# Kernel optimization log

Measured on AMD Instinct MI355X. Metric: run time of the kernel, lower is better.

The kernel has to match this reference:

```python
import jax, jax.numpy as jnp
import numpy as np

D = 768
H = 12
DK = D // H
FF = 3072
EPS = 1e-5


def layernorm(x, g, b):
    mu = jnp.mean(x, axis=-1, keepdims=True)
    var = jnp.mean((x - mu) ** 2, axis=-1, keepdims=True)
    return (x - mu) * jax.lax.rsqrt(var + EPS) * g + b


def setup_inputs() -> dict:
    key = jax.random.key(0)
    ks = jax.random.split(key, 12)
    B, S = 4, 2048
    s = 0.02
    return {
        "embedding": jax.random.normal(ks[0], (B, S, D), jnp.float32),
        "mask": jnp.ones((B, 1, 1, S), jnp.int32),
        "Wq": jax.random.normal(ks[1], (D, D), jnp.float32) * s,
        "bq": jnp.zeros((D,), jnp.float32),
        "Wk": jax.random.normal(ks[2], (D, D), jnp.float32) * s,
        "bk": jnp.zeros((D,), jnp.float32),
        "Wv": jax.random.normal(ks[3], (D, D), jnp.float32) * s,
        "bv": jnp.zeros((D,), jnp.float32),
        "Wo": jax.random.normal(ks[4], (D, D), jnp.float32) * s,
        "bo": jnp.zeros((D,), jnp.float32),
        "W1": jax.random.normal(ks[5], (D, FF), jnp.float32) * s,
        "b1": jnp.zeros((FF,), jnp.float32),
        "W2": jax.random.normal(ks[6], (FF, D), jnp.float32) * s,
        "b2": jnp.zeros((D,), jnp.float32),
        "ln_g": jnp.ones((D,), jnp.float32),
        "ln_b": jnp.zeros((D,), jnp.float32),
    }


def reference(embedding, mask, Wq, bq, Wk, bk, Wv, bv, Wo, bo, W1, b1, W2, b2, ln_g, ln_b):
    B, S, _ = embedding.shape
    # QKV projections -> [B, H, S, DK]
    def split_heads(t):
        return t.reshape(B, S, H, DK).transpose(0, 2, 1, 3)
    q = split_heads(embedding @ Wq + bq)
    k = split_heads(embedding @ Wk + bk)
    v = split_heads(embedding @ Wv + bv)
    scores = jnp.einsum("bhqd,bhkd->bhqk", q, k) / jnp.sqrt(jnp.float32(DK))
    scores = jnp.where(mask == 0, jnp.float32(-1e9), scores)
    weights = jax.nn.softmax(scores, axis=-1)  # dropout = identity (eval)
    context = jnp.einsum("bhqk,bhkd->bhqd", weights, v)
    context = context.transpose(0, 2, 1, 3).reshape(B, S, D)
    attn_out = context @ Wo + bo
    x = layernorm(attn_out + embedding, ln_g, ln_b)
    ff = jax.nn.relu(x @ W1 + b1) @ W2 + b2
    return layernorm(x + ff, ln_g, ln_b)
```

## Files before the change

kernel.cpp:

```cpp
#include <hip/hip_runtime.h>

#define D_MODEL 768
#define NHEADS  12
#define SEQ     2048
#define BATCH   4
#define FF_DIM  3072
#define NTOK    (BATCH * SEQ)

typedef short short8 __attribute__((ext_vector_type(8)));
typedef float f32x4 __attribute__((ext_vector_type(4)));
typedef float f32x16 __attribute__((ext_vector_type(16)));
typedef int int4v __attribute__((ext_vector_type(4)));
typedef int int2v __attribute__((ext_vector_type(2)));
typedef unsigned short ushort4v __attribute__((ext_vector_type(4)));
typedef float float4v __attribute__((ext_vector_type(4)));

__device__ __forceinline__ short f2bf(float x) {
  unsigned u = __builtin_bit_cast(unsigned, x);
  u += 0x7fffu + ((u >> 16) & 1u);
  return (short)(u >> 16);
}
__device__ __forceinline__ float bf2f(short x) {
  return __builtin_bit_cast(float, ((unsigned)(unsigned short)x) << 16);
}
__device__ __forceinline__ int cvtpk(float a, float b) {
  int r;
  asm("v_cvt_pk_bf16_f32 %0, %1, %2" : "=v"(r) : "v"(a), "v"(b));
  return r;
}
__device__ __forceinline__ float fexp2(float x) {
#if __has_builtin(__builtin_amdgcn_exp2f)
  return __builtin_amdgcn_exp2f(x);
#else
  return exp2f(x);
#endif
}
__device__ __forceinline__ float frcp(float x) {
#if __has_builtin(__builtin_amdgcn_rcpf)
  return __builtin_amdgcn_rcpf(x);
#else
  return 1.f / x;
#endif
}
__device__ __forceinline__ void gll16(const void* g, void* l) {
  __builtin_amdgcn_global_load_lds(
      (const __attribute__((address_space(1))) void*)g,
      (__attribute__((address_space(3))) void*)l, 16, 0, 0);
}

__device__ __forceinline__ void wt_tile(float (*T)[65], const float* __restrict__ W,
                                        short* __restrict__ Wt, int K, int N,
                                        int bx, int by, int t) {
  const int c = t & 63, rb = t >> 6;
  const int k0 = by * 64, n0 = bx * 64;
#pragma unroll
  for (int i = 0; i < 16; ++i) {
    const int r = rb * 16 + i;
    T[c][r] = W[(size_t)(k0 + r) * N + n0 + c];
  }
  __syncthreads();
#pragma unroll
  for (int j = 0; j < 16; ++j) {
    const int idx = t + j * 256;
    const int nl = idx >> 6, kl = idx & 63;
    Wt[(size_t)(n0 + nl) * K + k0 + kl] = f2bf(T[nl][kl]);
  }
}

__global__ __launch_bounds__(256) void prep(
    const float* __restrict__ Wq, const float* __restrict__ Wk, const float* __restrict__ Wv,
    const float* __restrict__ Wo, const float* __restrict__ W1, const float* __restrict__ W2,
    const float* __restrict__ bq, const float* __restrict__ bk, const float* __restrict__ bv,
    const float* __restrict__ emb,
    short* __restrict__ wqkvt, short* __restrict__ wot, short* __restrict__ w1t,
    short* __restrict__ w2t, float* __restrict__ bqkv, short* __restrict__ x0) {
  __shared__ float T[64][65];
  const int bi = blockIdx.x;
  const int t = threadIdx.x;
  if (bi < 432) {
    const int s = bi / 144, l = bi % 144;
    const float* W = (s == 0) ? Wq : (s == 1) ? Wk : Wv;
    wt_tile(T, W, wqkvt + (size_t)s * 768 * 768, 768, 768, l % 12, l / 12, t);
  } else if (bi < 576) {
    const int l = bi - 432;
    wt_tile(T, Wo, wot, 768, 768, l % 12, l / 12, t);
  } else if (bi < 1152) {
    const int l = bi - 576;
    wt_tile(T, W1, w1t, 768, 3072, l % 48, l / 48, t);
  } else if (bi < 1728) {
    const int l = bi - 1152;
    wt_tile(T, W2, w2t, 3072, 768, l % 12, l / 12, t);
  } else if (bi == 1728) {
#pragma unroll
    for (int j = 0; j < 9; ++j) {
      const int i = t + j * 256;
      bqkv[i] = (i < 768) ? bq[i] : (i < 1536) ? bk[i - 768] : bv[i - 1536];
    }
  } else {
    const int i = (bi - 1729) * 256 + t;
    float4v v = *(const float4v*)(emb + (size_t)i * 4);
    ushort4v p;
    p[0] = (unsigned short)f2bf(v[0]);
    p[1] = (unsigned short)f2bf(v[1]);
    p[2] = (unsigned short)f2bf(v[2]);
    p[3] = (unsigned short)f2bf(v[3]);
    *(ushort4v*)(x0 + (size_t)i * 4) = p;
  }
}

enum { EPI_QKV = 0, EPI_WO = 1, EPI_RELU = 2, EPI_FF = 3 };

template <int EPI>
__global__ __launch_bounds__(256) void gemm_bt(const short* __restrict__ A,
                                               const short* __restrict__ Bt,
                                               const float* __restrict__ bias,
                                               const float* __restrict__ extraF,
                                               const short* __restrict__ extraB,
                                               void* __restrict__ outp,
                                               int M, int N, int K) {
  __shared__ short As[128 * 64];
  __shared__ short Bs[128 * 64];
  const int tid = threadIdx.x;
  const int lane = tid & 63, wid = tid >> 6;
  const int wr = wid >> 1, wc = wid & 1;
  const int l16 = lane & 15, lg = lane >> 4;
  const int brow = blockIdx.y * 128, bcol = blockIdx.x * 128;

  f32x4 acc[4][4];
#pragma unroll
  for (int i = 0; i < 4; ++i)
#pragma unroll
    for (int j = 0; j < 4; ++j) acc[i][j] = (f32x4){0.f, 0.f, 0.f, 0.f};

  for (int kt = 0; kt < K; kt += 64) {
    __syncthreads();
#pragma unroll
    for (int i = 0; i < 4; ++i) {
      const int c = wid * 256 + i * 64 + lane;
      const int row = c >> 3;
      const int gc = (c & 7) ^ (row & 7);
      gll16(A + (size_t)(brow + row) * K + kt + gc * 8,
            (char*)As + (wid * 256 + i * 64) * 16);
      gll16(Bt + (size_t)(bcol + row) * K + kt + gc * 8,
            (char*)Bs + (wid * 256 + i * 64) * 16);
    }
    __syncthreads();
#pragma unroll
    for (int kc = 0; kc < 2; ++kc) {
      short8 af[4], bfr[4];
#pragma unroll
      for (int m = 0; m < 4; ++m) {
        const int row = wr * 64 + m * 16 + l16;
        const int ch = (kc * 4 + lg) ^ (row & 7);
        af[m] = *(const short8*)((const char*)As + row * 128 + ch * 16);
      }
#pragma unroll
      for (int n = 0; n < 4; ++n) {
        const int row = wc * 64 + n * 16 + l16;
        const int ch = (kc * 4 + lg) ^ (row & 7);
        bfr[n] = *(const short8*)((const char*)Bs + row * 128 + ch * 16);
      }
#pragma unroll
      for (int m = 0; m < 4; ++m)
#pragma unroll
        for (int n = 0; n < 4; ++n)
          acc[m][n] = __builtin_amdgcn_mfma_f32_16x16x32_bf16(af[m], bfr[n],
                                                              acc[m][n], 0, 0, 0);
    }
  }

  const int mbase = brow + wr * 64;
  const int nbase = bcol + wc * 64;

  if constexpr (EPI == EPI_QKV) {
    short* qb_ = (short*)outp;
    short* kb_ = qb_ + (size_t)NTOK * D_MODEL;
    short* vt_ = kb_ + (size_t)NTOK * D_MODEL;
    const int type = nbase / 768;
#pragma unroll
    for (int ni = 0; ni < 4; ++ni) {
      const int n = nbase + ni * 16 + l16;
      const float bv = bias[n];
      const int ncol = n - type * 768;
      const int h = ncol >> 6, dk = ncol & 63;
      if (type == 2) {
#pragma unroll
        for (int mi = 0; mi < 4; ++mi) {
          const int m0 = mbase + mi * 16 + lg * 4;
          const int bidx = m0 >> 11, s0 = m0 & 2047;
          ushort4v pk;
#pragma unroll
          for (int r = 0; r < 4; ++r) pk[r] = (unsigned short)f2bf(acc[mi][ni][r] + bv);
          *(ushort4v*)(vt_ + (((size_t)bidx * NHEADS + h) * 64 + dk) * SEQ + s0) = pk;
        }
      } else {
        short* o = (type == 0) ? qb_ : kb_;
        const float sc = (type == 0) ? 0.125f * 1.44269504f : 1.f;
#pragma unroll
        for (int mi = 0; mi < 4; ++mi) {
#pragma unroll
          for (int r = 0; r < 4; ++r) {
            const int m = mbase + mi * 16 + lg * 4 + r;
            const int bidx = m >> 11, sidx = m & 2047;
            o[(((size_t)bidx * NHEADS + h) * SEQ + sidx) * 64 + dk] =
                f2bf((acc[mi][ni][r] + bv) * sc);
          }
        }
      }
    }
  } else if constexpr (EPI == EPI_WO) {
    short* o = (short*)outp;
#pragma unroll
    for (int ni = 0; ni < 4; ++ni) {
      const int n = nbase + ni * 16 + l16;
      const float bv = bias[n];
#pragma unroll
      for (int mi = 0; mi < 4; ++mi)
#pragma unroll
        for (int r = 0; r < 4; ++r) {
          const int m = mbase + mi * 16 + lg * 4 + r;
          const size_t idx = (size_t)m * N + n;
          o[idx] = f2bf(acc[mi][ni][r] + bv + extraF[idx]);
        }
    }
  } else if constexpr (EPI == EPI_FF) {
    short* o = (short*)outp;
#pragma unroll
    for (int ni = 0; ni < 4; ++ni) {
      const int n = nbase + ni * 16 + l16;
      const float bv = bias[n];
#pragma unroll
      for (int mi = 0; mi < 4; ++mi)
#pragma unroll
        for (int r = 0; r < 4; ++r) {
          const int m = mbase + mi * 16 + lg * 4 + r;
          const size_t idx = (size_t)m * N + n;
          o[idx] = f2bf(acc[mi][ni][r] + bv + bf2f(extraB[idx]));
        }
    }
  } else {
    short* o = (short*)outp;
#pragma unroll
    for (int ni = 0; ni < 4; ++ni) {
      const int n = nbase + ni * 16 + l16;
      const float bv = bias[n];
#pragma unroll
      for (int mi = 0; mi < 4; ++mi)
#pragma unroll
        for (int r = 0; r < 4; ++r) {
          const int m = mbase + mi * 16 + lg * 4 + r;
          o[(size_t)m * N + n] = f2bf(fmaxf(acc[mi][ni][r] + bv, 0.f));
        }
    }
  }
}

__global__ __launch_bounds__(256) void attn_fa6(
    const short* __restrict__ Q,
    const short* __restrict__ Kb,
    const short* __restrict__ Vt,
    const int* __restrict__ mask,
    float* __restrict__ opart,
    float* __restrict__ lpart) {
  __shared__ short KsA[64 * 64], KsB[64 * 64];
  __shared__ short VsA[64 * 64], VsB[64 * 64];
  const int tid = threadIdx.x;
  const int lane = tid & 63, w = tid >> 6;
  const int l31 = lane & 31, hi = lane >> 5;

  const int i = blockIdx.x;
  const int r8 = i & 7, qq = i >> 3;
  const int bhz = ((qq >> 3) << 3) + r8;
  const int qblk = qq & 7;
  const int half = bhz / 48, bh = bhz % 48;
  const int b = bh / NHEADS;
  const int q0 = qblk * 256 + w * 64;
  const int kvbase = half * (SEQ / 2);

  const short* qpA = Q + ((size_t)bh * SEQ + q0 + l31) * 64;
  const short* qpB = qpA + 32 * 64;
  short8 qfA[4], qfB[4];
#pragma unroll
  for (int s = 0; s < 4; ++s) {
    qfA[s] = *(const short8*)(qpA + s * 16 + hi * 8);
    qfB[s] = *(const short8*)(qpB + s * 16 + hi * 8);
  }

  f32x16 o0a, o1a, o0b, o1b;
#pragma unroll
  for (int k = 0; k < 16; ++k) { o0a[k] = 0.f; o1a[k] = 0.f; o0b[k] = 0.f; o1b[k] = 0.f; }
  float lA = 0.f, lB = 0.f;

  auto stage = [&](short* Ksd, short* Vsd, int kv0) {
#pragma unroll
    for (int i2 = 0; i2 < 2; ++i2) {
      const int c = i2 * 256 + tid;
      const int row = c >> 3;
      const int gc = (c & 7) ^ (row & 7);
      gll16(Kb + ((size_t)bh * SEQ + kv0 + row) * 64 + gc * 8,
            (char*)Ksd + (i2 * 256 + w * 64) * 16);
      gll16(Vt + ((size_t)bh * 64 + row) * SEQ + kv0 + gc * 8,
            (char*)Vsd + (i2 * 256 + w * 64) * 16);
    }
  };

  stage(KsA, VsA, kvbase);
  __syncthreads();

  for (int t = 0; t < SEQ / 2 / 64; ++t) {
    const short* Ksc = (t & 1) ? KsB : KsA;
    const short* Vsc = (t & 1) ? VsB : VsA;

    const int mv = mask[(size_t)b * SEQ + kvbase + t * 64 + lane];
    const bool anym = __any(mv == 0);
    float ra = 0.f, rb_ = 0.f;
    short8 paA[4], paB[4];

#pragma unroll
    for (int ph = 0; ph < 2; ++ph) {
      f32x16 sa, sb;
#pragma unroll
      for (int k = 0; k < 16; ++k) { sa[k] = 0.f; sb[k] = 0.f; }
      const char* kr = (const char*)Ksc + (ph * 32 + l31) * 128;
#pragma unroll
      for (int slot = 0; slot < 4; ++slot) {
        const int ch = (slot * 2 + hi) ^ (l31 & 7);
        short8 kf = *(const short8*)(kr + ch * 16);
        sa = __builtin_amdgcn_mfma_f32_32x32x16_bf16(kf, qfA[slot], sa, 0, 0, 0);
        sb = __builtin_amdgcn_mfma_f32_32x32x16_bf16(kf, qfB[slot], sb, 0, 0, 0);
      }
      if (ph == 1 && t + 1 < SEQ / 2 / 64)
        stage((t & 1) ? KsA : KsB, (t & 1) ? VsA : VsB, kvbase + (t + 1) * 64);
      if (anym) {
#pragma unroll
        for (int r = 0; r < 16; ++r) {
          const int cr = ph * 32 + (r & 3) + 8 * (r >> 2) + 4 * hi;
          if (__shfl(mv, cr) == 0) { sa[r] = -1e9f; sb[r] = -1e9f; }
        }
      }
#pragma unroll
      for (int r = 0; r < 16; ++r) {
        sa[r] = fexp2(sa[r]);
        sb[r] = fexp2(sb[r]);
        ra += sa[r];
        rb_ += sb[r];
      }
#pragma unroll
      for (int ks = 0; ks < 2; ++ks) {
        const int rb0 = ks * 8;
#pragma unroll
        for (int g = 0; g < 2; ++g) {
          const f32x16& sc = g ? sb : sa;
          int x0_ = cvtpk(sc[rb0 + 0], sc[rb0 + 1]);
          int y0_ = cvtpk(sc[rb0 + 4], sc[rb0 + 5]);
          int x1_ = cvtpk(sc[rb0 + 2], sc[rb0 + 3]);
          int y1_ = cvtpk(sc[rb0 + 6], sc[rb0 + 7]);
          int4v pw;
#if __has_builtin(__builtin_amdgcn_permlane32_swap)
          int2v r0 = __builtin_amdgcn_permlane32_swap(x0_, y0_, false, false);
          int2v r1 = __builtin_amdgcn_permlane32_swap(x1_, y1_, false, false);
          pw[0] = r0[0]; pw[1] = r1[0]; pw[2] = r0[1]; pw[3] = r1[1];
#else
          const int ys0 = __shfl_xor(y0_, 32);
          const int xs0 = __shfl_xor(x0_, 32);
          const int ys1 = __shfl_xor(y1_, 32);
          const int xs1 = __shfl_xor(x1_, 32);
          pw[0] = hi ? ys0 : x0_;
          pw[1] = hi ? ys1 : x1_;
          pw[2] = hi ? y0_ : xs0;
          pw[3] = hi ? y1_ : xs1;
#endif
          const short8 pa = __builtin_bit_cast(short8, pw);
          if (g) paB[ph * 2 + ks] = pa; else paA[ph * 2 + ks] = pa;
        }
      }
    }
    lA += ra + __shfl_xor(ra, 32);
    lB += rb_ + __shfl_xor(rb_, 32);

#pragma unroll
    for (int vs = 0; vs < 4; ++vs) {
      const int vch = (vs * 2 + hi) ^ (l31 & 7);
      short8 vb0 = *(const short8*)((const char*)Vsc + l31 * 128 + vch * 16);
      short8 vb1 = *(const short8*)((const char*)Vsc + (32 + l31) * 128 + vch * 16);
      o0a = __builtin_amdgcn_mfma_f32_32x32x16_bf16(paA[vs], vb0, o0a, 0, 0, 0);
      o0b = __builtin_amdgcn_mfma_f32_32x32x16_bf16(paB[vs], vb0, o0b, 0, 0, 0);
      o1a = __builtin_amdgcn_mfma_f32_32x32x16_bf16(paA[vs], vb1, o1a, 0, 0, 0);
      o1b = __builtin_amdgcn_mfma_f32_32x32x16_bf16(paB[vs], vb1, o1b, 0, 0, 0);
    }
    __syncthreads();
  }

  float* opA = opart + ((size_t)half * BATCH * NHEADS + bh) * SEQ * 64;
#pragma unroll
  for (int r = 0; r < 16; ++r) {
    const int q = (r & 3) + 8 * (r >> 2) + 4 * hi;
    float* pa_ = opA + (size_t)(q0 + q) * 64;
    pa_[l31] = o0a[r];
    pa_[32 + l31] = o1a[r];
    float* pb_ = opA + (size_t)(q0 + 32 + q) * 64;
    pb_[l31] = o0b[r];
    pb_[32 + l31] = o1b[r];
  }
  if (lane < 32) {
    float* lp = lpart + (size_t)half * BATCH * NHEADS * SEQ + (size_t)bh * SEQ + q0;
    lp[l31] = lA;
    lp[32 + l31] = lB;
  }
}

__global__ __launch_bounds__(256) void attn_combine(const float* __restrict__ op,
                                                    const float* __restrict__ lp,
                                                    short* __restrict__ ctx) {
  const size_t HS = (size_t)BATCH * NHEADS * SEQ * 64;
  const int i4 = blockIdx.x * 256 + threadIdx.x;
  const size_t base = (size_t)i4 * 4;
  float4v a = *(const float4v*)(op + base);
  float4v c = *(const float4v*)(op + HS + base);
  const int row = (int)(base >> 6);
  const float inv = frcp(lp[row] + lp[BATCH * NHEADS * SEQ + row]);
  const int bh = row >> 11, q = row & 2047;
  const int b = bh / NHEADS, h = bh - b * NHEADS;
  const int dk = (int)(base & 63);
  ushort4v o;
#pragma unroll
  for (int j = 0; j < 4; ++j) o[j] = (unsigned short)f2bf((a[j] + c[j]) * inv);
  *(ushort4v*)(ctx + ((size_t)b * SEQ + q) * D_MODEL + h * 64 + dk) = o;
}

template <int OUT_F32>
__global__ __launch_bounds__(256) void ln_w(const short* __restrict__ y,
                                            const float* __restrict__ gw,
                                            const float* __restrict__ bw,
                                            float* __restrict__ of,
                                            short* __restrict__ ob) {
  const int lane = threadIdx.x & 63, w = threadIdx.x >> 6;
  const int row = blockIdx.x * 4 + w;
  const short* yr = y + (size_t)row * D_MODEL;
  short8 v8 = *(const short8*)(yr + lane * 8);
  ushort4v v4 = *(const ushort4v*)(yr + 512 + lane * 4);
  float f[12];
#pragma unroll
  for (int j = 0; j < 8; ++j) f[j] = bf2f(v8[j]);
#pragma unroll
  for (int j = 0; j < 4; ++j) f[8 + j] = bf2f((short)v4[j]);
  float s = 0.f, q = 0.f;
#pragma unroll
  for (int j = 0; j < 12; ++j) { s += f[j]; q += f[j] * f[j]; }
#pragma unroll
  for (int mm = 1; mm < 64; mm <<= 1) {
    s += __shfl_xor(s, mm);
    q += __shfl_xor(q, mm);
  }
  const float mu = s * (1.f / D_MODEL);
  const float rs = rsqrtf(q * (1.f / D_MODEL) - mu * mu + 1e-5f);
  float4v g0 = *(const float4v*)(gw + lane * 8);
  float4v g1 = *(const float4v*)(gw + lane * 8 + 4);
  float4v g2 = *(const float4v*)(gw + 512 + lane * 4);
  float4v b0 = *(const float4v*)(bw + lane * 8);
  float4v b1 = *(const float4v*)(bw + lane * 8 + 4);
  float4v b2 = *(const float4v*)(bw + 512 + lane * 4);
  float o[12];
#pragma unroll
  for (int j = 0; j < 4; ++j) o[j] = (f[j] - mu) * rs * g0[j] + b0[j];
#pragma unroll
  for (int j = 0; j < 4; ++j) o[4 + j] = (f[4 + j] - mu) * rs * g1[j] + b1[j];
#pragma unroll
  for (int j = 0; j < 4; ++j) o[8 + j] = (f[8 + j] - mu) * rs * g2[j] + b2[j];
  if constexpr (OUT_F32) {
    float* orow = of + (size_t)row * D_MODEL;
    float4v t0, t1, t2;
#pragma unroll
    for (int j = 0; j < 4; ++j) { t0[j] = o[j]; t1[j] = o[4 + j]; t2[j] = o[8 + j]; }
    *(float4v*)(orow + lane * 8) = t0;
    *(float4v*)(orow + lane * 8 + 4) = t1;
    *(float4v*)(orow + 512 + lane * 4) = t2;
  } else {
    short* orow = ob + (size_t)row * D_MODEL;
    ushort4v t0, t1, t2;
#pragma unroll
    for (int j = 0; j < 4; ++j) {
      t0[j] = (unsigned short)f2bf(o[j]);
      t1[j] = (unsigned short)f2bf(o[4 + j]);
      t2[j] = (unsigned short)f2bf(o[8 + j]);
    }
    *(ushort4v*)(orow + lane * 8) = t0;
    *(ushort4v*)(orow + lane * 8 + 4) = t1;
    *(ushort4v*)(orow + 512 + lane * 4) = t2;
  }
}

extern "C" void kernel_launch(void* const* d_in, const int* in_sizes, int n_in,
                              void* d_out, int out_size, void* d_ws, size_t ws_size,
                              hipStream_t stream) {
  const float* emb = (const float*)d_in[0];
  const int* mask = (const int*)d_in[1];
  const float* Wq = (const float*)d_in[2];
  const float* bq = (const float*)d_in[3];
  const float* Wk = (const float*)d_in[4];
  const float* bk = (const float*)d_in[5];
  const float* Wv = (const float*)d_in[6];
  const float* bv = (const float*)d_in[7];
  const float* Wo = (const float*)d_in[8];
  const float* bo = (const float*)d_in[9];
  const float* W1 = (const float*)d_in[10];
  const float* b1 = (const float*)d_in[11];
  const float* W2 = (const float*)d_in[12];
  const float* b2 = (const float*)d_in[13];
  const float* lng = (const float*)d_in[14];
  const float* lnb = (const float*)d_in[15];

  char* ws = (char*)d_ws;
  size_t off = 0;
  auto alloc = [&](size_t bytes) -> char* {
    char* p = ws + off;
    off = (off + bytes + 255) & ~(size_t)255;
    return p;
  };
  const size_t DD = (size_t)D_MODEL * D_MODEL;
  const size_t DF = (size_t)D_MODEL * FF_DIM;
  const size_t TD = (size_t)NTOK * D_MODEL;
  const size_t TF = (size_t)NTOK * FF_DIM;

  short* wqkvt = (short*)alloc(3 * DD * 2);
  short* wot = (short*)alloc(DD * 2);
  short* w1t = (short*)alloc(DF * 2);
  short* w2t = (short*)alloc(DF * 2);
  float* bqkv = (float*)alloc(2304 * 4);
  short* x0 = (short*)alloc(TD * 2);
  short* qkv = (short*)alloc(3 * TD * 2);
  short* aresb = (short*)alloc(TD * 2);
  short* xbf = (short*)alloc(TD * 2);
  short* hbf = (short*)alloc(TF * 2);
  short* ffresb = (short*)alloc(TD * 2);
  float* lpart = (float*)alloc(2 * (size_t)BATCH * NHEADS * SEQ * 4);
  short* qb = qkv;
  short* kb = qkv + TD;
  short* vtb = qkv + 2 * TD;
  short* ctx = x0;
  float* opart = (float*)hbf;

  prep<<<dim3(1729 + (int)(TD / 1024)), 256, 0, stream>>>(
      Wq, Wk, Wv, Wo, W1, W2, bq, bk, bv, emb, wqkvt, wot, w1t, w2t, bqkv, x0);
  gemm_bt<EPI_QKV><<<dim3(18, 64), 256, 0, stream>>>(
      x0, wqkvt, bqkv, nullptr, nullptr, qkv, NTOK, 3 * D_MODEL, D_MODEL);
  attn_fa6<<<dim3(768), 256, 0, stream>>>(qb, kb, vtb, mask, opart, lpart);
  attn_combine<<<dim3((int)((size_t)BATCH * NHEADS * SEQ * 64 / 4 / 256)), 256, 0, stream>>>(
      opart, lpart, ctx);
  gemm_bt<EPI_WO><<<dim3(6, 64), 256, 0, stream>>>(
      ctx, wot, bo, emb, nullptr, aresb, NTOK, D_MODEL, D_MODEL);
  ln_w<0><<<dim3(NTOK / 4), 256, 0, stream>>>(aresb, lng, lnb, nullptr, xbf);
  gemm_bt<EPI_RELU><<<dim3(24, 64), 256, 0, stream>>>(
      xbf, w1t, b1, nullptr, nullptr, hbf, NTOK, FF_DIM, D_MODEL);
  gemm_bt<EPI_FF><<<dim3(6, 64), 256, 0, stream>>>(
      hbf, w2t, b2, nullptr, xbf, ffresb, NTOK, D_MODEL, FF_DIM);
  ln_w<1><<<dim3(NTOK / 4), 256, 0, stream>>>(ffresb, lng, lnb, (float*)d_out, nullptr);
}
```

Before: 299.0 us.

## Add 128x64 GEMM kernel for N=768 projections and tune attention priorities

Adds a new gemm_bn64 kernel with 128x64 tiles for the Wo and W2 GEMMs (N=768), doubling the block count from 384 to 768 to fill more CUs. In the attention kernel, MFMA sections are wrapped in s_setprio to favor matrix issue, and the per-tile cross-half row-sum shuffle is moved to after the loop. The smaller tile raises occupancy on the 256-CU device at the cost of less reuse per block and no double-buffered loads.

```diff
diff --git a/kernel.cpp b/kernel.cpp
--- a/kernel.cpp
+++ b/kernel.cpp
@@ -208,36 +208,6 @@
         }
       }
     }
-  } else if constexpr (EPI == EPI_WO) {
-    short* o = (short*)outp;
-#pragma unroll
-    for (int ni = 0; ni < 4; ++ni) {
-      const int n = nbase + ni * 16 + l16;
-      const float bv = bias[n];
-#pragma unroll
-      for (int mi = 0; mi < 4; ++mi)
-#pragma unroll
-        for (int r = 0; r < 4; ++r) {
-          const int m = mbase + mi * 16 + lg * 4 + r;
-          const size_t idx = (size_t)m * N + n;
-          o[idx] = f2bf(acc[mi][ni][r] + bv + extraF[idx]);
-        }
-    }
-  } else if constexpr (EPI == EPI_FF) {
-    short* o = (short*)outp;
-#pragma unroll
-    for (int ni = 0; ni < 4; ++ni) {
-      const int n = nbase + ni * 16 + l16;
-      const float bv = bias[n];
-#pragma unroll
-      for (int mi = 0; mi < 4; ++mi)
-#pragma unroll
-        for (int r = 0; r < 4; ++r) {
-          const int m = mbase + mi * 16 + lg * 4 + r;
-          const size_t idx = (size_t)m * N + n;
-          o[idx] = f2bf(acc[mi][ni][r] + bv + bf2f(extraB[idx]));
-        }
-    }
   } else {
     short* o = (short*)outp;
 #pragma unroll
@@ -252,6 +222,90 @@
           o[(size_t)m * N + n] = f2bf(fmaxf(acc[mi][ni][r] + bv, 0.f));
         }
     }
+  }
+}
+
+template <int EPI>
+__global__ __launch_bounds__(256) void gemm_bn64(const short* __restrict__ A,
+                                                 const short* __restrict__ Bt,
+                                                 const float* __restrict__ bias,
+                                                 const float* __restrict__ extraF,
+                                                 const short* __restrict__ extraB,
+                                                 void* __restrict__ outp,
+                                                 int M, int N, int K) {
+  __shared__ short As[128 * 64];
+  __shared__ short Bs[64 * 64];
+  const int tid = threadIdx.x;
+  const int lane = tid & 63, wid = tid >> 6;
+  const int l16 = lane & 15, lg = lane >> 4;
+  const int brow = blockIdx.y * 128, bcol = blockIdx.x * 64;
+
+  f32x4 acc[2][4];
+#pragma unroll
+  for (int i = 0; i < 2; ++i)
+#pragma unroll
+    for (int j = 0; j < 4; ++j) acc[i][j] = (f32x4){0.f, 0.f, 0.f, 0.f};
+
+  for (int kt = 0; kt < K; kt += 64) {
+    __syncthreads();
+#pragma unroll
+    for (int i = 0; i < 4; ++i) {
+      const int c = wid * 256 + i * 64 + lane;
+      const int row = c >> 3;
+      const int gc = (c & 7) ^ (row & 7);
+      gll16(A + (size_t)(brow + row) * K + kt + gc * 8,
+            (char*)As + (wid * 256 + i * 64) * 16);
+    }
+#pragma unroll
+    for (int i = 0; i < 2; ++i) {
+      const int c = i * 256 + tid;
+      const int row = c >> 3;
+      const int gc = (c & 7) ^ (row & 7);
+      gll16(Bt + (size_t)(bcol + row) * K + kt + gc * 8,
+            (char*)Bs + (i * 256 + wid * 64) * 16);
+    }
+    __syncthreads();
+#pragma unroll
+    for (int kc = 0; kc < 2; ++kc) {
+      short8 af[2], bfr[4];
+#pragma unroll
+      for (int m = 0; m < 2; ++m) {
+        const int row = wid * 32 + m * 16 + l16;
+        const int ch = (kc * 4 + lg) ^ (row & 7);
+        af[m] = *(const short8*)((const char*)As + row * 128 + ch * 16);
+      }
+#pragma unroll
+      for (int n = 0; n < 4; ++n) {
+        const int row = n * 16 + l16;
+        const int ch = (kc * 4 + lg) ^ (row & 7);
+        bfr[n] = *(const short8*)((const char*)Bs + row * 128 + ch * 16);
+      }
+#pragma unroll
+      for (int m = 0; m < 2; ++m)
+#pragma unroll
+        for (int n = 0; n < 4; ++n)
+          acc[m][n] = __builtin_amdgcn_mfma_f32_16x16x32_bf16(af[m], bfr[n],
+                                                              acc[m][n], 0, 0, 0);
+    }
+  }
+
+  const int mbase = brow + wid * 32;
+#pragma unroll
+  for (int ni = 0; ni < 4; ++ni) {
+    const int n = bcol + ni * 16 + l16;
+    const float bv = bias[n];
+#pragma unroll
+    for (int mi = 0; mi < 2; ++mi)
+#pragma unroll
+      for (int r = 0; r < 4; ++r) {
+        const int m = mbase + mi * 16 + lg * 4 + r;
+        const size_t idx = (size_t)m * N + n;
+        if constexpr (EPI == EPI_WO) {
+          ((short*)outp)[idx] = f2bf(acc[mi][ni][r] + bv + extraF[idx]);
+        } else {
+          ((short*)outp)[idx] = f2bf(acc[mi][ni][r] + bv + bf2f(extraB[idx]));
+        }
+      }
   }
 }
 
@@ -313,7 +367,6 @@
 
     const int mv = mask[(size_t)b * SEQ + kvbase + t * 64 + lane];
     const bool anym = __any(mv == 0);
-    float ra = 0.f, rb_ = 0.f;
     short8 paA[4], paB[4];
 
 #pragma unroll
@@ -322,6 +375,7 @@
 #pragma unroll
       for (int k = 0; k < 16; ++k) { sa[k] = 0.f; sb[k] = 0.f; }
       const char* kr = (const char*)Ksc + (ph * 32 + l31) * 128;
+      __builtin_amdgcn_s_setprio(1);
 #pragma unroll
       for (int slot = 0; slot < 4; ++slot) {
         const int ch = (slot * 2 + hi) ^ (l31 & 7);
@@ -329,6 +383,7 @@
         sa = __builtin_amdgcn_mfma_f32_32x32x16_bf16(kf, qfA[slot], sa, 0, 0, 0);
         sb = __builtin_amdgcn_mfma_f32_32x32x16_bf16(kf, qfB[slot], sb, 0, 0, 0);
       }
+      __builtin_amdgcn_s_setprio(0);
       if (ph == 1 && t + 1 < SEQ / 2 / 64)
         stage((t & 1) ? KsA : KsB, (t & 1) ? VsA : VsB, kvbase + (t + 1) * 64);
       if (anym) {
@@ -342,8 +397,8 @@
       for (int r = 0; r < 16; ++r) {
         sa[r] = fexp2(sa[r]);
         sb[r] = fexp2(sb[r]);
-        ra += sa[r];
-        rb_ += sb[r];
+        lA += sa[r];
+        lB += sb[r];
       }
 #pragma unroll
       for (int ks = 0; ks < 2; ++ks) {
@@ -375,9 +430,8 @@
         }
       }
     }
-    lA += ra + __shfl_xor(ra, 32);
-    lB += rb_ + __shfl_xor(rb_, 32);
-
+
+    __builtin_amdgcn_s_setprio(1);
 #pragma unroll
     for (int vs = 0; vs < 4; ++vs) {
       const int vch = (vs * 2 + hi) ^ (l31 & 7);
@@ -388,8 +442,12 @@
       o1a = __builtin_amdgcn_mfma_f32_32x32x16_bf16(paA[vs], vb1, o1a, 0, 0, 0);
       o1b = __builtin_amdgcn_mfma_f32_32x32x16_bf16(paB[vs], vb1, o1b, 0, 0, 0);
     }
+    __builtin_amdgcn_s_setprio(0);
     __syncthreads();
   }
+
+  lA += __shfl_xor(lA, 32);
+  lB += __shfl_xor(lB, 32);
 
   float* opA = opart + ((size_t)half * BATCH * NHEADS + bh) * SEQ * 64;
 #pragma unroll
@@ -547,12 +605,12 @@
   attn_fa6<<<dim3(768), 256, 0, stream>>>(qb, kb, vtb, mask, opart, lpart);
   attn_combine<<<dim3((int)((size_t)BATCH * NHEADS * SEQ * 64 / 4 / 256)), 256, 0, stream>>>(
       opart, lpart, ctx);
-  gemm_bt<EPI_WO><<<dim3(6, 64), 256, 0, stream>>>(
+  gemm_bn64<EPI_WO><<<dim3(12, 64), 256, 0, stream>>>(
       ctx, wot, bo, emb, nullptr, aresb, NTOK, D_MODEL, D_MODEL);
   ln_w<0><<<dim3(NTOK / 4), 256, 0, stream>>>(aresb, lng, lnb, nullptr, xbf);
   gemm_bt<EPI_RELU><<<dim3(24, 64), 256, 0, stream>>>(
       xbf, w1t, b1, nullptr, nullptr, hbf, NTOK, FF_DIM, D_MODEL);
-  gemm_bt<EPI_FF><<<dim3(6, 64), 256, 0, stream>>>(
+  gemm_bn64<EPI_FF><<<dim3(12, 64), 256, 0, stream>>>(
       hbf, w2t, b2, nullptr, xbf, ffresb, NTOK, D_MODEL, FF_DIM);
   ln_w<1><<<dim3(NTOK / 4), 256, 0, stream>>>(ffresb, lng, lnb, (float*)d_out, nullptr);
 }
```

Measured after the change: 289.3 us. 3.2% less time.
